# Kernel tuning notes

Hardware: AMD Instinct MI355X
Metric: run time of the kernel (lower is better)

Reference implementation:

```python
import math
import jax, jax.numpy as jnp
import numpy as np


def _alibi_slopes(n_heads: int) -> np.ndarray:
    def pow2_slopes(n):
        start = 2 ** (-2 ** (-(math.log2(n) - 3)))
        return [start * (start ** i) for i in range(n)]
    if n_heads & (n_heads - 1) == 0:
        slopes = pow2_slopes(n_heads)
    else:
        closest = 2 ** math.floor(math.log2(n_heads))
        slopes = pow2_slopes(closest)
        extra_base = 2 ** (-2 ** (-(math.log2(2 * closest) - 3)))
        slopes.extend(extra_base * (extra_base ** i) for i in range(n_heads - closest))
        slopes = slopes[:n_heads]
    return np.asarray(slopes, dtype=np.float32)


def setup_inputs() -> dict:
    B, T, C, H = 2, 2048, 768, 12
    key = jax.random.key(0)
    ks = jax.random.split(key, 6)
    return {
        "x_norm_for_qk": jax.random.normal(ks[0], (B, T, C), jnp.float32),
        "xt_current_for_v": jax.random.normal(ks[1], (B, T, C), jnp.float32),
        "W_attn": jax.random.normal(ks[2], (2 * C, C), jnp.float32) * 0.02,  # nn.Linear weight [out,in]
        "b_attn": jnp.zeros((2 * C,), jnp.float32),
        "v_tmp": jax.random.normal(ks[3], (H, H), jnp.float32) * 0.02,
        "proj_tmp": jax.random.normal(ks[4], (H, H), jnp.float32) * 0.02,
    }


def reference(x_norm_for_qk, xt_current_for_v, W_attn, b_attn, v_tmp, proj_tmp):
    B, T, C = x_norm_for_qk.shape
    H = v_tmp.shape[0]
    hd = C // H

    # Q,K projection: Linear(C -> 2C), then split.
    qk = x_norm_for_qk @ W_attn.T + b_attn  # [B,T,2C]
    q, k = jnp.split(qk, 2, axis=-1)
    q = q.reshape(B, T, H, hd).transpose(0, 2, 1, 3)  # [B,H,T,hd]
    k = k.reshape(B, T, H, hd).transpose(0, 2, 1, 3)

    # Kronecker-lifted V: block (i,j) of the CxC matrix is v_tmp[i,j]*I(hd),
    # so applying it mixes only across heads per head-dim channel.
    xt = xt_current_for_v.reshape(B, T, H, hd)
    v = jnp.einsum("ij,btjd->btid", v_tmp, xt).transpose(0, 2, 1, 3)  # [B,H,T,hd]

    scale = 1.0 / math.sqrt(hd)
    scores = jnp.einsum("bhqd,bhkd->bhqk", q, k) * scale  # [B,H,T,T]

    # ALiBi bias with causal mask (-inf above diagonal).
    slopes = jnp.asarray(_alibi_slopes(H))  # [H]
    pos = jnp.arange(T, dtype=jnp.float32)
    rel = pos[None, :] - pos[:, None]  # [T,T], memory - context
    causal = pos[None, :] <= pos[:, None]
    bias = jnp.where(causal[None], slopes[:, None, None] * rel[None], -jnp.inf)  # [H,T,T]
    scores = scores + bias[None]

    att = jax.nn.softmax(scores, axis=-1)  # dropout p=0 -> identity
    y = jnp.einsum("bhqk,bhkd->bhqd", att, v)  # [B,H,T,hd]
    y = y.transpose(0, 2, 1, 3)  # [B,T,H,hd]

    # Kronecker-lifted output projection.
    y = jnp.einsum("ij,btjd->btid", proj_tmp, y)
    return y.reshape(B, T, C)
```

## Files before the change

### kernel.cpp

```cpp
#include <hip/hip_runtime.h>
#include <hip/hip_bf16.h>
#include <math.h>

#define TSEQ 2048
#define CDIM 768
#define NH   12
#define HD   64

typedef __attribute__((ext_vector_type(8))) short bf16x8;
typedef __attribute__((ext_vector_type(4))) float f32x4;

union Bf8 { bf16x8 v; __hip_bfloat16 e[8]; };

__constant__ float c_slopes2[12] = {
    0.72134752f, 0.36067376f, 0.18033688f, 0.09016844f,
    0.04508422f, 0.02254211f, 0.011271055f, 0.0056355275f,
    1.02015692f, 0.72134752f, 0.51007846f, 0.36067376f
};
#define M2 4.3280851f
#define QSCALE 0.18033688f
#define EXP2F(x) __builtin_amdgcn_exp2f(x)

__device__ __forceinline__ unsigned pack2(float lo, float hi) {
    union { __hip_bfloat162 b; unsigned u; } cv;
    cv.b = __float22bfloat162_rn(make_float2(lo, hi));
    return cv.u;
}
__device__ __forceinline__ unsigned short bf16bits(float x) {
    union { __hip_bfloat16 b; unsigned short s; } cv;
    cv.b = __float2bfloat16(x);
    return cv.s;
}
__device__ __forceinline__ void gload16(const __hip_bfloat16* g, char* l) {
    __builtin_amdgcn_global_load_lds(
        (const __attribute__((address_space(1))) void*)g,
        (__attribute__((address_space(3))) void*)l, 16, 0, 0);
}

#define MFMA16(a, b, c) __builtin_amdgcn_mfma_f32_16x16x32_bf16(a, b, c, 0, 0, 0)
#define WAITV8 asm volatile("s_waitcnt vmcnt(8)" ::: "memory");
#define WAITV0 asm volatile("s_waitcnt vmcnt(0)" ::: "memory");

__global__ __launch_bounds__(512) void gemm_qk(
    const float* __restrict__ X,
    const float* __restrict__ W,
    const float* __restrict__ bias,
    __hip_bfloat16* __restrict__ Qb,
    __hip_bfloat16* __restrict__ Kb)
{
    __shared__ alignas(16) __hip_bfloat16 As[128][40];
    __shared__ alignas(16) __hip_bfloat16 Bs[128][40];

    const int tid  = threadIdx.x;
    const int lane = tid & 63;
    const int w    = tid >> 6;
    const int lg   = lane >> 4;
    const int lc   = lane & 15;
    const int m0   = blockIdx.y * 128;
    const int n0   = blockIdx.x * 128;
    const int m0w  = (w >> 2) * 64;
    const int n0w  = (w & 3) * 32;

    const int srow = tid >> 2;
    const int scol = (tid & 3) * 8;

    f32x4 acc[4][2] = {};

    for (int k0 = 0; k0 < CDIM; k0 += 32) {
        __syncthreads();
        {
            const float* xp = X + (size_t)(m0 + srow) * CDIM + k0 + scol;
            const float* wp = W + (size_t)(n0 + srow) * CDIM + k0 + scol;
            float4 a0 = *(const float4*)(xp);
            float4 a1 = *(const float4*)(xp + 4);
            float4 b0 = *(const float4*)(wp);
            float4 b1 = *(const float4*)(wp + 4);
            Bf8 av, bv;
            av.e[0]=__float2bfloat16(a0.x); av.e[1]=__float2bfloat16(a0.y);
            av.e[2]=__float2bfloat16(a0.z); av.e[3]=__float2bfloat16(a0.w);
            av.e[4]=__float2bfloat16(a1.x); av.e[5]=__float2bfloat16(a1.y);
            av.e[6]=__float2bfloat16(a1.z); av.e[7]=__float2bfloat16(a1.w);
            bv.e[0]=__float2bfloat16(b0.x); bv.e[1]=__float2bfloat16(b0.y);
            bv.e[2]=__float2bfloat16(b0.z); bv.e[3]=__float2bfloat16(b0.w);
            bv.e[4]=__float2bfloat16(b1.x); bv.e[5]=__float2bfloat16(b1.y);
            bv.e[6]=__float2bfloat16(b1.z); bv.e[7]=__float2bfloat16(b1.w);
            *(bf16x8*)&As[srow][scol] = av.v;
            *(bf16x8*)&Bs[srow][scol] = bv.v;
        }
        __syncthreads();

        bf16x8 af[4], bfr[2];
        #pragma unroll
        for (int mt = 0; mt < 4; ++mt)
            af[mt] = *(const bf16x8*)&As[m0w + mt*16 + lc][lg*8];
        #pragma unroll
        for (int nt = 0; nt < 2; ++nt)
            bfr[nt] = *(const bf16x8*)&Bs[n0w + nt*16 + lc][lg*8];
        #pragma unroll
        for (int mt = 0; mt < 4; ++mt)
            #pragma unroll
            for (int nt = 0; nt < 2; ++nt)
                acc[mt][nt] = MFMA16(af[mt], bfr[nt], acc[mt][nt]);
    }

    #pragma unroll
    for (int mt = 0; mt < 4; ++mt) {
        #pragma unroll
        for (int nt = 0; nt < 2; ++nt) {
            int n  = n0 + n0w + nt*16 + lc;
            float bv = bias[n];
            #pragma unroll
            for (int r = 0; r < 4; ++r) {
                int m = m0 + m0w + mt*16 + lg*4 + r;
                float v = acc[mt][nt][r] + bv;
                int b = m >> 11, t = m & (TSEQ-1);
                if (n < CDIM) {
                    int h = n >> 6, dd = n & 63;
                    Qb[(((size_t)(b*NH + h))*TSEQ + t)*HD + dd] = __float2bfloat16(v * QSCALE);
                } else {
                    int n2 = n - CDIM;
                    int h = n2 >> 6, dd = n2 & 63;
                    Kb[(((size_t)(b*NH + h))*TSEQ + t)*HD + dd] = __float2bfloat16(v);
                }
            }
        }
    }
}

__global__ __launch_bounds__(256) void vmix(
    const float* __restrict__ XT, const float* __restrict__ vtmp,
    __hip_bfloat16* __restrict__ Vb)
{
    __shared__ float vm[144];
    if (threadIdx.x < 144) vm[threadIdx.x] = vtmp[threadIdx.x];
    __syncthreads();
    int idx = blockIdx.x * 256 + threadIdx.x;
    int dd = idx & 63;
    int bt = idx >> 6;
    int t = bt & (TSEQ-1), b = bt >> 11;
    float xv[12];
    #pragma unroll
    for (int j = 0; j < 12; ++j) xv[j] = XT[(size_t)bt*CDIM + j*64 + dd];
    #pragma unroll
    for (int i = 0; i < 12; ++i) {
        float s = 0.f;
        #pragma unroll
        for (int j = 0; j < 12; ++j) s += vm[i*12+j] * xv[j];
        Vb[(((size_t)(b*NH + i))*TSEQ + t)*HD + dd] = __float2bfloat16(s);
    }
}

__global__ __launch_bounds__(256) void vtrans(
    const __hip_bfloat16* __restrict__ Vb, __hip_bfloat16* __restrict__ Vt)
{
    __shared__ __hip_bfloat16 Ls[64][65];
    const int bh = blockIdx.y;
    const int t0 = blockIdx.x * 64;
    const int tid = threadIdx.x;
    const int r8 = tid >> 3;
    const int c8 = (tid & 7) * 8;

    #pragma unroll
    for (int it = 0; it < 2; ++it) {
        int t = it*32 + r8;
        Bf8 v; v.v = *(const bf16x8*)(Vb + ((size_t)bh*TSEQ + t0 + t)*HD + c8);
        #pragma unroll
        for (int j = 0; j < 8; ++j) Ls[t][c8 + j] = v.e[j];
    }
    __syncthreads();
    #pragma unroll
    for (int it = 0; it < 2; ++it) {
        int d = it*32 + r8;
        Bf8 v;
        #pragma unroll
        for (int j = 0; j < 8; ++j) v.e[j] = Ls[c8 + j][d];
        int kb = (t0 + c8) >> 5;
        int ko = (t0 + c8) & 31;
        *(bf16x8*)(Vt + (size_t)bh*(HD*TSEQ) + kb*2048 + d*32 + ko) = v.v;
    }
}

__global__ __launch_bounds__(128, 4) void attn7(
    const __hip_bfloat16* __restrict__ Qb,
    const __hip_bfloat16* __restrict__ Kb,
    const __hip_bfloat16* __restrict__ Vt,
    __hip_bfloat16* __restrict__ Y)
{
    __shared__ alignas(16) char kstage[2][2][4096];
    __shared__ alignas(16) float comb[2][16][68];
    __shared__ float lcomb[2][16];

    const int tid  = threadIdx.x;
    const int lane = tid & 63;
    const int w    = tid >> 6;
    const int lg   = lane >> 4;
    const int lc   = lane & 15;

    const int id  = blockIdx.x;
    const int id2 = (id & 7) * 96 + (id >> 3);
    const int bx  = id2 & 31;
    const int bh  = id2 >> 5;

    const float slope = c_slopes2[bh % NH];
    const __hip_bfloat16* Qp = Qb + (size_t)bh * TSEQ * HD;
    const __hip_bfloat16* Kp = Kb + (size_t)bh * TSEQ * HD;
    const __hip_bfloat16* Vp = Vt + (size_t)bh * (HD * TSEQ);

    const int kRow = lane >> 3;
    const int kCh  = ((lane & 7) ^ kRow) * 8;

    char* myK = &kstage[w][0][0];
    const float slgl  = slope * (float)(lg * 4);
    const float slp16 = slope * 16.0f;
    const int   s01   = lc + ((lg & 1) << 5);
    const int   s23   = s01 + 16;
    const bool  hiK   = (lg >= 2);

#define ISSK(K0, BUF) do {                                                      \
    char* db_ = myK + (BUF)*4096;                                               \
    const __hip_bfloat16* kg_ = Kp + (size_t)((K0) + kRow)*HD + kCh;            \
    gload16(kg_,         db_);                                                  \
    gload16(kg_ +  8*HD, db_ + 1024);                                           \
    gload16(kg_ + 16*HD, db_ + 2048);                                           \
    gload16(kg_ + 24*HD, db_ + 3072);                                           \
} while (0);

#define VLOADX(P0, P1, P2, P3, K0) do {                                         \
    const __hip_bfloat16* vb_ = Vp + (size_t)((K0) >> 5) * 2048 + lc*32 + lg*8; \
    P0 = *(const bf16x8*)(vb_);                                                 \
    P1 = *(const bf16x8*)(vb_ + 512);                                           \
    P2 = *(const bf16x8*)(vb_ + 1024);                                          \
    P3 = *(const bf16x8*)(vb_ + 1536);                                          \
} while (0);

#define SHUF(P_, x0, x1, x2, x3)                                                \
    {                                                                           \
        int t00 = __shfl((int)x0, s01), t02 = __shfl((int)x2, s01);             \
        int t10 = __shfl((int)x1, s01), t12 = __shfl((int)x3, s01);             \
        int t20 = __shfl((int)x0, s23), t22 = __shfl((int)x2, s23);             \
        int t30 = __shfl((int)x1, s23), t32 = __shfl((int)x3, s23);             \
        P_.u[0] = hiK ? (unsigned)t02 : (unsigned)t00;                          \
        P_.u[1] = hiK ? (unsigned)t12 : (unsigned)t10;                          \
        P_.u[2] = hiK ? (unsigned)t22 : (unsigned)t20;                          \
        P_.u[3] = hiK ? (unsigned)t32 : (unsigned)t30;                          \
    }

#define CONS(K0C, BUF, V0_, V1_, V2_, V3_) do {                                 \
    const char* bK_ = myK + (BUF)*4096;                                         \
    const int swzk_ = lc & 7;                                                   \
    const char* kr0_ = bK_ + lc*128;                                            \
    const char* kr1_ = bK_ + (16 + lc)*128;                                     \
    bf16x8 k0lo = *(const bf16x8*)(kr0_ + (((lg    ) ^ swzk_) << 4));           \
    bf16x8 k0hi = *(const bf16x8*)(kr0_ + (((lg + 4) ^ swzk_) << 4));           \
    bf16x8 k1lo = *(const bf16x8*)(kr1_ + (((lg    ) ^ swzk_) << 4));           \
    bf16x8 k1hi = *(const bf16x8*)(kr1_ + (((lg + 4) ^ swzk_) << 4));           \
    f32x4 s0a = {}, s0b = {}, s1a = {}, s1b = {};                               \
    s0a = MFMA16(k0lo, qfa0, s0a); s0a = MFMA16(k0hi, qfa1, s0a);               \
    s0b = MFMA16(k0lo, qfb0, s0b); s0b = MFMA16(k0hi, qfb1, s0b);               \
    s1a = MFMA16(k1lo, qfa0, s1a); s1a = MFMA16(k1hi, qfa1, s1a);               \
    s1b = MFMA16(k1lo, qfb0, s1b); s1b = MFMA16(k1hi, qfb1, s1b);               \
    float base0_ = fmaf((float)(K0C), slope, slgl);                             \
    float pa0[4], pa1[4], pb0[4], pb1[4];                                       \
    _Pragma("unroll")                                                           \
    for (int r = 0; r < 4; ++r) {                                               \
        float bk_  = base0_ + slope * (float)r;                                 \
        float bk1_ = bk_ + slp16;                                               \
        int kk0_ = (K0C) + lg*4 + r, kk1_ = kk0_ + 16;                          \
        float e0a = EXP2F(s0a[r] + (bk_  - eqa));                               \
        float e1a = EXP2F(s1a[r] + (bk1_ - eqa));                               \
        float e0b = EXP2F(s0b[r] + (bk_  - eqb));                               \
        float e1b = EXP2F(s1b[r] + (bk1_ - eqb));                               \
        pa0[r] = (kk0_ <= qia) ? e0a : 0.f;                                     \
        pa1[r] = (kk1_ <= qia) ? e1a : 0.f;                                     \
        pb0[r] = (kk0_ <= qib) ? e0b : 0.f;                                     \
        pb1[r] = (kk1_ <= qib) ? e1b : 0.f;                                     \
        lsa += pa0[r] + pa1[r];                                                 \
        lsb += pb0[r] + pb1[r];                                                 \
    }                                                                           \
    unsigned a0_ = pack2(pa0[0], pa0[1]), a1_ = pack2(pa0[2], pa0[3]);          \
    unsigned a2_ = pack2(pa1[0], pa1[1]), a3_ = pack2(pa1[2], pa1[3]);          \
    unsigned b0_ = pack2(pb0[0], pb0[1]), b1_ = pack2(pb0[2], pb0[3]);          \
    unsigned b2_ = pack2(pb1[0], pb1[1]), b3_ = pack2(pb1[2], pb1[3]);          \
    union { unsigned u[4]; bf16x8 v; } PA_, PB_;                                \
    SHUF(PA_, a0_, a1_, a2_, a3_)                                               \
    SHUF(PB_, b0_, b1_, b2_, b3_)                                               \
    Oa[0] = MFMA16(V0_, PA_.v, Oa[0]); Ob[0] = MFMA16(V0_, PB_.v, Ob[0]);       \
    Oa[1] = MFMA16(V1_, PA_.v, Oa[1]); Ob[1] = MFMA16(V1_, PB_.v, Ob[1]);       \
    Oa[2] = MFMA16(V2_, PA_.v, Oa[2]); Ob[2] = MFMA16(V2_, PB_.v, Ob[2]);       \
    Oa[3] = MFMA16(V3_, PA_.v, Oa[3]); Ob[3] = MFMA16(V3_, PB_.v, Ob[3]);       \
} while (0);

    auto runMember = [&](int qb, bool first) {
        const int q0m = qb * 32;
        const int qia = q0m + lc;
        const int qib = q0m + 16 + lc;
        const float eqa = slope * (float)qia + M2;
        const float eqb = slope * (float)qib + M2;

        bf16x8 qfa0 = *(const bf16x8*)(Qp + (size_t)qia * HD + lg*8);
        bf16x8 qfa1 = *(const bf16x8*)(Qp + (size_t)qia * HD + 32 + lg*8);
        bf16x8 qfb0 = *(const bf16x8*)(Qp + (size_t)qib * HD + lg*8);
        bf16x8 qfb1 = *(const bf16x8*)(Qp + (size_t)qib * HD + 32 + lg*8);

        f32x4 Oa[4] = {}; f32x4 Ob[4] = {};
        float lsa = 0.f, lsb = 0.f;

        const int myN = (qb >= w) ? ((qb - w) >> 1) + 1 : 0;

        bf16x8 vA0, vA1, vA2, vA3, vB0, vB1, vB2, vB3;

        if (myN > 0) {
            ISSK(w*32, 0)
            VLOADX(vA0, vA1, vA2, vA3, w*32)
            int j = 0;
            while (true) {
                if (j + 1 < myN) {
                    const int kn = (w + 2*(j+1)) * 32;
                    ISSK(kn, (j+1) & 1)
                    VLOADX(vB0, vB1, vB2, vB3, kn)
                    WAITV8
                } else { WAITV0 }
                CONS((w + 2*j)*32, j & 1, vA0, vA1, vA2, vA3)
                ++j; if (j >= myN) break;
                if (j + 1 < myN) {
                    const int kn = (w + 2*(j+1)) * 32;
                    ISSK(kn, (j+1) & 1)
                    VLOADX(vA0, vA1, vA2, vA3, kn)
                    WAITV8
                } else { WAITV0 }
                CONS((w + 2*j)*32, j & 1, vB0, vB1, vB2, vB3)
                ++j; if (j >= myN) break;
            }
        }

        lsa += __shfl_xor(lsa, 16); lsa += __shfl_xor(lsa, 32);
        lsb += __shfl_xor(lsb, 16); lsb += __shfl_xor(lsb, 32);

        if (!first) __syncthreads();
        if (w == 0) {
            #pragma unroll
            for (int dt = 0; dt < 4; ++dt)
                *(f32x4*)&comb[0][lc][dt*16 + lg*4] = Ob[dt];
            if (lane < 16) lcomb[0][lane] = lsb;
        } else {
            #pragma unroll
            for (int dt = 0; dt < 4; ++dt)
                *(f32x4*)&comb[1][lc][dt*16 + lg*4] = Oa[dt];
            if (lane < 16) lcomb[1][lane] = lsa;
        }
        __syncthreads();

        const int q = q0m + w*16 + lc;
        float lt  = ((w == 0) ? lsa : lsb) + lcomb[1 ^ w][lc];
        float inv = 1.0f / lt;
        #pragma unroll
        for (int dt = 0; dt < 4; ++dt) {
            f32x4 o = (w == 0) ? Oa[dt] : Ob[dt];
            o += *(const f32x4*)&comb[1 ^ w][lc][dt*16 + lg*4];
            ushort4 u;
            u.x = bf16bits(o[0] * inv);
            u.y = bf16bits(o[1] * inv);
            u.z = bf16bits(o[2] * inv);
            u.w = bf16bits(o[3] * inv);
            *(ushort4*)(Y + ((size_t)bh*TSEQ + q)*HD + dt*16 + lg*4) = u;
        }
    };

    runMember(bx, true);
    runMember(63 - bx, false);

#undef ISSK
#undef VLOADX
#undef SHUF
#undef CONS
}

__global__ __launch_bounds__(256) void projmix(
    const __hip_bfloat16* __restrict__ Y, const float* __restrict__ ptmp,
    float* __restrict__ Out)
{
    __shared__ float pm[144];
    if (threadIdx.x < 144) pm[threadIdx.x] = ptmp[threadIdx.x];
    __syncthreads();
    int idx = blockIdx.x * 256 + threadIdx.x;
    int dd = idx & 63;
    int bt = idx >> 6;
    int t = bt & (TSEQ-1), b = bt >> 11;
    float yv[12];
    #pragma unroll
    for (int j = 0; j < 12; ++j)
        yv[j] = __bfloat162float(Y[(((size_t)(b*NH + j))*TSEQ + t)*HD + dd]);
    #pragma unroll
    for (int i = 0; i < 12; ++i) {
        float s = 0.f;
        #pragma unroll
        for (int j = 0; j < 12; ++j) s += pm[i*12+j] * yv[j];
        Out[(size_t)bt*CDIM + i*64 + dd] = s;
    }
}

extern "C" void kernel_launch(void* const* d_in, const int* in_sizes, int n_in,
                              void* d_out, int out_size, void* d_ws, size_t ws_size,
                              hipStream_t stream) {
    (void)in_sizes; (void)n_in; (void)out_size; (void)ws_size;
    const float* X    = (const float*)d_in[0];
    const float* XT   = (const float*)d_in[1];
    const float* W    = (const float*)d_in[2];
    const float* bias = (const float*)d_in[3];
    const float* vtmp = (const float*)d_in[4];
    const float* ptmp = (const float*)d_in[5];
    float* Out = (float*)d_out;

    char* ws = (char*)d_ws;
    const size_t BHTD = (size_t)2 * NH * TSEQ * HD;
    __hip_bfloat16* Qb = (__hip_bfloat16*)ws;
    __hip_bfloat16* Kb = (__hip_bfloat16*)(ws + BHTD*2);
    __hip_bfloat16* Vb = (__hip_bfloat16*)(ws + BHTD*4);
    __hip_bfloat16* Vt = (__hip_bfloat16*)(ws + BHTD*6);
    __hip_bfloat16* Yb = (__hip_bfloat16*)(ws + BHTD*8);

    gemm_qk<<<dim3(12, 32), 512, 0, stream>>>(X, W, bias, Qb, Kb);
    vmix<<<1024, 256, 0, stream>>>(XT, vtmp, Vb);
    vtrans<<<dim3(32, 24), 256, 0, stream>>>(Vb, Vt);
    attn7<<<768, 128, 0, stream>>>(Qb, Kb, Vt, Yb);
    projmix<<<1024, 256, 0, stream>>>(Yb, ptmp, Out);
}
```

Before: 93.32 us.

## Store K pre-swizzled for MFMA, load directly to registers, split keys over 4 waves

The QK GEMM epilogue now writes K in a fragment-ready tiled layout, so the attention kernel loads K straight into registers and drops the LDS staging and explicit vmcnt waits. The attention kernel goes from 2 to 4 waves per block, each taking every fourth 32-key tile, and partial outputs and row sums are reduced across the four waves through shared memory. This is meant to cut LDS traffic and raise per-block parallelism. The cost is scattered 2-byte global stores in the GEMM epilogue, lower occupancy per block (launch bounds 256,3), and a larger cross-wave reduction.

```diff
diff --git a/kernel.cpp b/kernel.cpp
--- a/kernel.cpp
+++ b/kernel.cpp
@@ -31,22 +31,15 @@
     cv.b = __float2bfloat16(x);
     return cv.s;
 }
-__device__ __forceinline__ void gload16(const __hip_bfloat16* g, char* l) {
-    __builtin_amdgcn_global_load_lds(
-        (const __attribute__((address_space(1))) void*)g,
-        (__attribute__((address_space(3))) void*)l, 16, 0, 0);
-}
 
 #define MFMA16(a, b, c) __builtin_amdgcn_mfma_f32_16x16x32_bf16(a, b, c, 0, 0, 0)
-#define WAITV8 asm volatile("s_waitcnt vmcnt(8)" ::: "memory");
-#define WAITV0 asm volatile("s_waitcnt vmcnt(0)" ::: "memory");
 
 __global__ __launch_bounds__(512) void gemm_qk(
     const float* __restrict__ X,
     const float* __restrict__ W,
     const float* __restrict__ bias,
     __hip_bfloat16* __restrict__ Qb,
-    __hip_bfloat16* __restrict__ Kb)
+    __hip_bfloat16* __restrict__ Kt)
 {
     __shared__ alignas(16) __hip_bfloat16 As[128][40];
     __shared__ alignas(16) __hip_bfloat16 Bs[128][40];
@@ -120,7 +113,12 @@
                 } else {
                     int n2 = n - CDIM;
                     int h = n2 >> 6, dd = n2 & 63;
-                    Kb[(((size_t)(b*NH + h))*TSEQ + t)*HD + dd] = __float2bfloat16(v);
+                    int bh_ = b*NH + h;
+                    int kb = t >> 5, tt = t & 31;
+                    int j  = ((tt >> 4) << 1) + (dd >> 5);
+                    int ln = (((dd >> 3) & 3) << 4) + (tt & 15);
+                    Kt[((size_t)(bh_*64 + kb))*2048 + j*512 + ln*8 + (dd & 7)] =
+                        __float2bfloat16(v);
                 }
             }
         }
@@ -180,15 +178,14 @@
     }
 }
 
-__global__ __launch_bounds__(128, 4) void attn7(
+__global__ __launch_bounds__(256, 3) void attn8(
     const __hip_bfloat16* __restrict__ Qb,
-    const __hip_bfloat16* __restrict__ Kb,
+    const __hip_bfloat16* __restrict__ Kt,
     const __hip_bfloat16* __restrict__ Vt,
     __hip_bfloat16* __restrict__ Y)
 {
-    __shared__ alignas(16) char kstage[2][2][4096];
-    __shared__ alignas(16) float comb[2][16][68];
-    __shared__ float lcomb[2][16];
+    __shared__ float Osh[4][2][64][20];
+    __shared__ float Lsh[4][2][16];
 
     const int tid  = threadIdx.x;
     const int lane = tid & 63;
@@ -203,34 +200,23 @@
 
     const float slope = c_slopes2[bh % NH];
     const __hip_bfloat16* Qp = Qb + (size_t)bh * TSEQ * HD;
-    const __hip_bfloat16* Kp = Kb + (size_t)bh * TSEQ * HD;
+    const __hip_bfloat16* Kp = Kt + (size_t)bh * 64 * 2048;
     const __hip_bfloat16* Vp = Vt + (size_t)bh * (HD * TSEQ);
 
-    const int kRow = lane >> 3;
-    const int kCh  = ((lane & 7) ^ kRow) * 8;
-
-    char* myK = &kstage[w][0][0];
     const float slgl  = slope * (float)(lg * 4);
     const float slp16 = slope * 16.0f;
     const int   s01   = lc + ((lg & 1) << 5);
     const int   s23   = s01 + 16;
     const bool  hiK   = (lg >= 2);
 
-#define ISSK(K0, BUF) do {                                                      \
-    char* db_ = myK + (BUF)*4096;                                               \
-    const __hip_bfloat16* kg_ = Kp + (size_t)((K0) + kRow)*HD + kCh;            \
-    gload16(kg_,         db_);                                                  \
-    gload16(kg_ +  8*HD, db_ + 1024);                                           \
-    gload16(kg_ + 16*HD, db_ + 2048);                                           \
-    gload16(kg_ + 24*HD, db_ + 3072);                                           \
-} while (0);
-
-#define VLOADX(P0, P1, P2, P3, K0) do {                                         \
-    const __hip_bfloat16* vb_ = Vp + (size_t)((K0) >> 5) * 2048 + lc*32 + lg*8; \
-    P0 = *(const bf16x8*)(vb_);                                                 \
-    P1 = *(const bf16x8*)(vb_ + 512);                                           \
-    P2 = *(const bf16x8*)(vb_ + 1024);                                          \
-    P3 = *(const bf16x8*)(vb_ + 1536);                                          \
+    bf16x8 kA0, kA1, kA2, kA3, kB0, kB1, kB2, kB3;
+
+#define LOADK(S, TI) do {                                                       \
+    const __hip_bfloat16* kp_ = Kp + (size_t)(TI)*2048 + lane*8;                \
+    k##S##0 = *(const bf16x8*)(kp_);                                            \
+    k##S##1 = *(const bf16x8*)(kp_ + 512);                                      \
+    k##S##2 = *(const bf16x8*)(kp_ + 1024);                                     \
+    k##S##3 = *(const bf16x8*)(kp_ + 1536);                                     \
 } while (0);
 
 #define SHUF(P_, x0, x1, x2, x3)                                                \
@@ -245,27 +231,25 @@
         P_.u[3] = hiK ? (unsigned)t32 : (unsigned)t30;                          \
     }
 
-#define CONS(K0C, BUF, V0_, V1_, V2_, V3_) do {                                 \
-    const char* bK_ = myK + (BUF)*4096;                                         \
-    const int swzk_ = lc & 7;                                                   \
-    const char* kr0_ = bK_ + lc*128;                                            \
-    const char* kr1_ = bK_ + (16 + lc)*128;                                     \
-    bf16x8 k0lo = *(const bf16x8*)(kr0_ + (((lg    ) ^ swzk_) << 4));           \
-    bf16x8 k0hi = *(const bf16x8*)(kr0_ + (((lg + 4) ^ swzk_) << 4));           \
-    bf16x8 k1lo = *(const bf16x8*)(kr1_ + (((lg    ) ^ swzk_) << 4));           \
-    bf16x8 k1hi = *(const bf16x8*)(kr1_ + (((lg + 4) ^ swzk_) << 4));           \
+#define CONS(TI, S) do {                                                        \
+    const int K0C = (TI) * 32;                                                  \
+    const __hip_bfloat16* vb_ = Vp + (size_t)(TI)*2048 + lc*32 + lg*8;          \
+    bf16x8 v0_ = *(const bf16x8*)(vb_);                                         \
+    bf16x8 v1_ = *(const bf16x8*)(vb_ + 512);                                   \
+    bf16x8 v2_ = *(const bf16x8*)(vb_ + 1024);                                  \
+    bf16x8 v3_ = *(const bf16x8*)(vb_ + 1536);                                  \
     f32x4 s0a = {}, s0b = {}, s1a = {}, s1b = {};                               \
-    s0a = MFMA16(k0lo, qfa0, s0a); s0a = MFMA16(k0hi, qfa1, s0a);               \
-    s0b = MFMA16(k0lo, qfb0, s0b); s0b = MFMA16(k0hi, qfb1, s0b);               \
-    s1a = MFMA16(k1lo, qfa0, s1a); s1a = MFMA16(k1hi, qfa1, s1a);               \
-    s1b = MFMA16(k1lo, qfb0, s1b); s1b = MFMA16(k1hi, qfb1, s1b);               \
-    float base0_ = fmaf((float)(K0C), slope, slgl);                             \
+    s0a = MFMA16(k##S##0, qfa0, s0a); s0a = MFMA16(k##S##1, qfa1, s0a);         \
+    s0b = MFMA16(k##S##0, qfb0, s0b); s0b = MFMA16(k##S##1, qfb1, s0b);         \
+    s1a = MFMA16(k##S##2, qfa0, s1a); s1a = MFMA16(k##S##3, qfa1, s1a);         \
+    s1b = MFMA16(k##S##2, qfb0, s1b); s1b = MFMA16(k##S##3, qfb1, s1b);         \
+    float base0_ = fmaf((float)K0C, slope, slgl);                               \
     float pa0[4], pa1[4], pb0[4], pb1[4];                                       \
     _Pragma("unroll")                                                           \
     for (int r = 0; r < 4; ++r) {                                               \
         float bk_  = base0_ + slope * (float)r;                                 \
         float bk1_ = bk_ + slp16;                                               \
-        int kk0_ = (K0C) + lg*4 + r, kk1_ = kk0_ + 16;                          \
+        int kk0_ = K0C + lg*4 + r, kk1_ = kk0_ + 16;                            \
         float e0a = EXP2F(s0a[r] + (bk_  - eqa));                               \
         float e1a = EXP2F(s1a[r] + (bk1_ - eqa));                               \
         float e0b = EXP2F(s0b[r] + (bk_  - eqb));                               \
@@ -284,10 +268,10 @@
     union { unsigned u[4]; bf16x8 v; } PA_, PB_;                                \
     SHUF(PA_, a0_, a1_, a2_, a3_)                                               \
     SHUF(PB_, b0_, b1_, b2_, b3_)                                               \
-    Oa[0] = MFMA16(V0_, PA_.v, Oa[0]); Ob[0] = MFMA16(V0_, PB_.v, Ob[0]);       \
-    Oa[1] = MFMA16(V1_, PA_.v, Oa[1]); Ob[1] = MFMA16(V1_, PB_.v, Ob[1]);       \
-    Oa[2] = MFMA16(V2_, PA_.v, Oa[2]); Ob[2] = MFMA16(V2_, PB_.v, Ob[2]);       \
-    Oa[3] = MFMA16(V3_, PA_.v, Oa[3]); Ob[3] = MFMA16(V3_, PB_.v, Ob[3]);       \
+    Oa[0] = MFMA16(v0_, PA_.v, Oa[0]); Ob[0] = MFMA16(v0_, PB_.v, Ob[0]);       \
+    Oa[1] = MFMA16(v1_, PA_.v, Oa[1]); Ob[1] = MFMA16(v1_, PB_.v, Ob[1]);       \
+    Oa[2] = MFMA16(v2_, PA_.v, Oa[2]); Ob[2] = MFMA16(v2_, PB_.v, Ob[2]);       \
+    Oa[3] = MFMA16(v3_, PA_.v, Oa[3]); Ob[3] = MFMA16(v3_, PB_.v, Ob[3]);       \
 } while (0);
 
     auto runMember = [&](int qb, bool first) {
@@ -305,30 +289,17 @@
         f32x4 Oa[4] = {}; f32x4 Ob[4] = {};
         float lsa = 0.f, lsb = 0.f;
 
-        const int myN = (qb >= w) ? ((qb - w) >> 1) + 1 : 0;
-
-        bf16x8 vA0, vA1, vA2, vA3, vB0, vB1, vB2, vB3;
+        const int myN = (qb >= w) ? ((qb - w) >> 2) + 1 : 0;
 
         if (myN > 0) {
-            ISSK(w*32, 0)
-            VLOADX(vA0, vA1, vA2, vA3, w*32)
+            LOADK(A, w)
             int j = 0;
             while (true) {
-                if (j + 1 < myN) {
-                    const int kn = (w + 2*(j+1)) * 32;
-                    ISSK(kn, (j+1) & 1)
-                    VLOADX(vB0, vB1, vB2, vB3, kn)
-                    WAITV8
-                } else { WAITV0 }
-                CONS((w + 2*j)*32, j & 1, vA0, vA1, vA2, vA3)
+                if (j + 1 < myN) LOADK(B, w + 4*(j+1))
+                CONS(w + 4*j, A)
                 ++j; if (j >= myN) break;
-                if (j + 1 < myN) {
-                    const int kn = (w + 2*(j+1)) * 32;
-                    ISSK(kn, (j+1) & 1)
-                    VLOADX(vA0, vA1, vA2, vA3, kn)
-                    WAITV8
-                } else { WAITV0 }
-                CONS((w + 2*j)*32, j & 1, vB0, vB1, vB2, vB3)
+                if (j + 1 < myN) LOADK(A, w + 4*(j+1))
+                CONS(w + 4*j, B)
                 ++j; if (j >= myN) break;
             }
         }
@@ -337,40 +308,39 @@
         lsb += __shfl_xor(lsb, 16); lsb += __shfl_xor(lsb, 32);
 
         if (!first) __syncthreads();
-        if (w == 0) {
+        #pragma unroll
+        for (int dt = 0; dt < 4; ++dt) {
+            *(f32x4*)&Osh[w][0][lane][dt*4] = Oa[dt];
+            *(f32x4*)&Osh[w][1][lane][dt*4] = Ob[dt];
+        }
+        if (lane < 16) {
+            Lsh[w][0][lane] = lsa;
+            Lsh[w][1][lane] = lsb;
+        }
+        __syncthreads();
+
+        #pragma unroll
+        for (int h = 0; h < 2; ++h) {
+            f32x4 o = (h == 0) ? Oa[w] : Ob[w];
             #pragma unroll
-            for (int dt = 0; dt < 4; ++dt)
-                *(f32x4*)&comb[0][lc][dt*16 + lg*4] = Ob[dt];
-            if (lane < 16) lcomb[0][lane] = lsb;
-        } else {
-            #pragma unroll
-            for (int dt = 0; dt < 4; ++dt)
-                *(f32x4*)&comb[1][lc][dt*16 + lg*4] = Oa[dt];
-            if (lane < 16) lcomb[1][lane] = lsa;
-        }
-        __syncthreads();
-
-        const int q = q0m + w*16 + lc;
-        float lt  = ((w == 0) ? lsa : lsb) + lcomb[1 ^ w][lc];
-        float inv = 1.0f / lt;
-        #pragma unroll
-        for (int dt = 0; dt < 4; ++dt) {
-            f32x4 o = (w == 0) ? Oa[dt] : Ob[dt];
-            o += *(const f32x4*)&comb[1 ^ w][lc][dt*16 + lg*4];
+            for (int w2 = 0; w2 < 4; ++w2)
+                if (w2 != w) o += *(const f32x4*)&Osh[w2][h][lane][w*4];
+            float lt = Lsh[0][h][lc] + Lsh[1][h][lc] + Lsh[2][h][lc] + Lsh[3][h][lc];
+            float inv = 1.0f / lt;
+            int q = q0m + h*16 + lc;
             ushort4 u;
             u.x = bf16bits(o[0] * inv);
             u.y = bf16bits(o[1] * inv);
             u.z = bf16bits(o[2] * inv);
             u.w = bf16bits(o[3] * inv);
-            *(ushort4*)(Y + ((size_t)bh*TSEQ + q)*HD + dt*16 + lg*4) = u;
+            *(ushort4*)(Y + ((size_t)bh*TSEQ + q)*HD + w*16 + lg*4) = u;
         }
     };
 
     runMember(bx, true);
     runMember(63 - bx, false);
 
-#undef ISSK
-#undef VLOADX
+#undef LOADK
 #undef SHUF
 #undef CONS
 }
@@ -414,14 +384,14 @@
     char* ws = (char*)d_ws;
     const size_t BHTD = (size_t)2 * NH * TSEQ * HD;
     __hip_bfloat16* Qb = (__hip_bfloat16*)ws;
-    __hip_bfloat16* Kb = (__hip_bfloat16*)(ws + BHTD*2);
+    __hip_bfloat16* Kt = (__hip_bfloat16*)(ws + BHTD*2);
     __hip_bfloat16* Vb = (__hip_bfloat16*)(ws + BHTD*4);
     __hip_bfloat16* Vt = (__hip_bfloat16*)(ws + BHTD*6);
     __hip_bfloat16* Yb = (__hip_bfloat16*)(ws + BHTD*8);
 
-    gemm_qk<<<dim3(12, 32), 512, 0, stream>>>(X, W, bias, Qb, Kb);
+    gemm_qk<<<dim3(12, 32), 512, 0, stream>>>(X, W, bias, Qb, Kt);
     vmix<<<1024, 256, 0, stream>>>(XT, vtmp, Vb);
     vtrans<<<dim3(32, 24), 256, 0, stream>>>(Vb, Vt);
-    attn7<<<768, 128, 0, stream>>>(Qb, Kb, Vt, Yb);
+    attn8<<<768, 256, 0, stream>>>(Qb, Kt, Vt, Yb);
     projmix<<<1024, 256, 0, stream>>>(Yb, ptmp, Out);
 }
```

Measured after the change: 84.57 us. 9.4% less time.
